# Optimization experiments

Hardware: AMD Instinct MI355X
Metric: run time of the kernel (lower is better)

The kernel has to match this reference:

```python
import jax, jax.numpy as jnp
import numpy as np

B, S, D, DOUT, E = 2, 2048, 1024, 1024, 8
DH = 4 * D  # expert hidden size


def setup_inputs() -> dict:
    key = jax.random.key(0)
    ks = jax.random.split(key, 7)
    sc = lambda *sh: 1.0 / np.sqrt(sh[-2]) if len(sh) >= 2 else 0.02
    return {
        "x": jax.random.normal(ks[0], (B, S, D), jnp.float32),
        "Wg": jax.random.normal(ks[1], (D, E), jnp.float32) / np.sqrt(D),
        "bg": jnp.zeros((E,), jnp.float32),
        "W1": jax.random.normal(ks[2], (E, D, DH), jnp.float32) / np.sqrt(D),
        "b1": jax.random.normal(ks[3], (E, DH), jnp.float32) * 0.02,
        "W2": jax.random.normal(ks[4], (E, DH, DOUT), jnp.float32) / np.sqrt(DH),
        "b2": jax.random.normal(ks[5], (E, DOUT), jnp.float32) * 0.02,
    }


def reference(x, Wg, bg, W1, b1, W2, b2):
    # x: [B, S, D] -> flatten tokens (chunking over seq in the original is
    # math-neutral: routing and expert MLP are per-token).
    Bb, Ss, Dd = x.shape
    xt = x.reshape(-1, Dd)                       # [T, D]
    # Gate: softmax then argmax (top-1 routing, output NOT scaled by gate prob)
    gates = jax.nn.softmax(xt @ Wg + bg, axis=-1)  # [T, E]
    sel = jnp.argmax(gates, axis=-1)               # [T]
    nE = W1.shape[0]
    out = jnp.zeros((xt.shape[0], W2.shape[-1]), x.dtype)
    # Grouped expert MLP expressed as masked dense loop over the small fixed
    # expert count (jit-friendly; a fused gather-grouped-GEMM-scatter kernel
    # is the optimization target).
    for e in range(nE):
        h = jax.nn.gelu(xt @ W1[e] + b1[e], approximate=False)  # [T, 4D]
        ye = h @ W2[e] + b2[e]                                  # [T, DOUT]
        out = jnp.where((sel == e)[:, None], ye, out)
    return out.reshape(Bb, Ss, -1)
```

## Files before the change

### kernel.cpp

```cpp
#include <hip/hip_runtime.h>
#include <hip/hip_bf16.h>
#include <math.h>

#define T_TOK 4096
#define DIM   1024
#define NEXP  8
#define DHID  4096
#define NDOUT 1024
#define BM    128
#define MAXTILES 40

typedef short bf16x8 __attribute__((ext_vector_type(8)));
typedef float f32x4 __attribute__((ext_vector_type(4)));

__device__ __forceinline__ unsigned short f2bf(float f) {
  unsigned u = __float_as_uint(f);
  u += 0x7fffu + ((u >> 16) & 1u);
  return (unsigned short)(u >> 16);
}
__device__ __forceinline__ unsigned pack2bf(float a, float b) {
  return (unsigned)f2bf(a) | ((unsigned)f2bf(b) << 16);
}
__device__ __forceinline__ void gl_lds16(const void* g, void* l) {
  __builtin_amdgcn_global_load_lds(
      (const __attribute__((address_space(1))) void*)g,
      (__attribute__((address_space(3))) void*)l, 16, 0, 0);
}
__device__ __forceinline__ float gelu_fast(float h) {
  float z  = 0.79788456080286536f * (h + 0.044715f * h * h * h);
  float az = fabsf(z);
  float et = __expf(-2.0f * az);
  float th = (1.0f - et) / (1.0f + et);
  th = copysignf(th, z);
  return 0.5f * h * (1.0f + th);
}

__global__ __launch_bounds__(256)
void gate_kernel(const float* __restrict__ x, const float* __restrict__ Wg,
                 const float* __restrict__ bg, int* __restrict__ sel,
                 unsigned short* __restrict__ xbf) {
  int lane = threadIdx.x & 63;
  int wid  = threadIdx.x >> 6;
  int t = blockIdx.x * 4 + wid;
  if (t >= T_TOK) return;
  const float* xr = x + (size_t)t * DIM;
  unsigned short* xbr = xbf + (size_t)t * DIM;
  double acc[NEXP];
#pragma unroll
  for (int e = 0; e < NEXP; e++) acc[e] = 0.0;
#pragma unroll
  for (int j = 0; j < 4; j++) {
    int d0 = j * 256 + lane * 4;
    float4 v = *(const float4*)(xr + d0);
    uint2 p; p.x = pack2bf(v.x, v.y); p.y = pack2bf(v.z, v.w);
    *(uint2*)(xbr + d0) = p;
    float xs[4] = {v.x, v.y, v.z, v.w};
#pragma unroll
    for (int i = 0; i < 4; i++) {
      const float4* wr = reinterpret_cast<const float4*>(Wg + (size_t)(d0 + i) * NEXP);
      float4 w0 = wr[0], w1 = wr[1];
      double xv = (double)xs[i];
      acc[0] += xv * (double)w0.x;
      acc[1] += xv * (double)w0.y;
      acc[2] += xv * (double)w0.z;
      acc[3] += xv * (double)w0.w;
      acc[4] += xv * (double)w1.x;
      acc[5] += xv * (double)w1.y;
      acc[6] += xv * (double)w1.z;
      acc[7] += xv * (double)w1.w;
    }
  }
#pragma unroll
  for (int off = 32; off >= 1; off >>= 1) {
#pragma unroll
    for (int e = 0; e < NEXP; e++) acc[e] += __shfl_down(acc[e], off);
  }
  if (lane == 0) {
    double best = acc[0] + (double)bg[0];
    int bi = 0;
#pragma unroll
    for (int e = 1; e < NEXP; e++) {
      double v = acc[e] + (double)bg[e];
      if (v > best) { best = v; bi = e; }
    }
    sel[t] = bi;
  }
}

__global__ void zero_kernel(int* __restrict__ counts) {
  if (threadIdx.x < NEXP) counts[threadIdx.x] = 0;
}

__global__ void hist_kernel(const int* __restrict__ sel, int* __restrict__ counts) {
  __shared__ int lc[NEXP];
  if (threadIdx.x < NEXP) lc[threadIdx.x] = 0;
  __syncthreads();
  int t = blockIdx.x * 256 + threadIdx.x;
  atomicAdd(&lc[sel[t]], 1);
  __syncthreads();
  if (threadIdx.x < NEXP) atomicAdd(&counts[threadIdx.x], lc[threadIdx.x]);
}

__global__ void plan_kernel(const int* __restrict__ counts, int* __restrict__ base,
                            int* __restrict__ cursor, int* __restrict__ tileExpert,
                            int* __restrict__ tilePos, int* __restrict__ tileRows,
                            int* __restrict__ ntiles) {
  if (threadIdx.x == 0) {
    int acc = 0, nt = 0;
    for (int e = 0; e < NEXP; e++) {
      base[e] = acc; cursor[e] = acc;
      int c = counts[e];
      for (int j = 0; j < c; j += BM) {
        tileExpert[nt] = e;
        tilePos[nt]    = acc + j;
        int rem = c - j;
        tileRows[nt]   = rem < BM ? rem : BM;
        nt++;
      }
      acc += c;
    }
    *ntiles = nt;
  }
}

__global__ void scatter_kernel(const int* __restrict__ sel, int* __restrict__ cursor,
                               int* __restrict__ list) {
  __shared__ int lcnt[NEXP];
  __shared__ int lbase[NEXP];
  int tid = threadIdx.x;
  if (tid < NEXP) lcnt[tid] = 0;
  __syncthreads();
  int t = blockIdx.x * 256 + tid;
  int e = sel[t];
  int lpos = atomicAdd(&lcnt[e], 1);
  __syncthreads();
  if (tid < NEXP) lbase[tid] = atomicAdd(&cursor[tid], lcnt[tid]);
  __syncthreads();
  list[lbase[e] + lpos] = t;
}

__global__ __launch_bounds__(256)
void transpose_tile_kernel(const float* __restrict__ in, unsigned short* __restrict__ out,
                           int K, int N) {
  int nb = blockIdx.x, kb = blockIdx.y, e = blockIdx.z;
  const float* inp = in + (size_t)e * K * N;
  __shared__ unsigned short lds[128][72];
  int tx = threadIdx.x;
  int kloc = tx >> 5;
  int n4   = (tx & 31) << 2;
#pragma unroll
  for (int p = 0; p < 8; p++) {
    int k = p * 8 + kloc;
    float4 v = *(const float4*)(inp + (size_t)(kb * 64 + k) * N + nb * 128 + n4);
    lds[n4 + 0][k] = f2bf(v.x);
    lds[n4 + 1][k] = f2bf(v.y);
    lds[n4 + 2][k] = f2bf(v.z);
    lds[n4 + 3][k] = f2bf(v.w);
  }
  __syncthreads();
  char* tile = (char*)(out + (((size_t)e * gridDim.x + nb) * gridDim.y + kb) * 8192);
  int r  = tx >> 1;
  int kc0 = (tx & 1) * 32;
#pragma unroll
  for (int c = 0; c < 4; c++) {
    int kc = kc0 + c * 8;
    uint4 v = *(const uint4*)&lds[r][kc];
    *(uint4*)(tile + r * 128 + ((2 * kc) ^ ((r & 7) << 4))) = v;
  }
}


__global__ __launch_bounds__(256)
void gemm1_kernel(const unsigned short* __restrict__ xbf, const unsigned short* __restrict__ W1T,
                  const float* __restrict__ b1, const int* __restrict__ list,
                  const int* __restrict__ tileExpert, const int* __restrict__ tilePos,
                  const int* __restrict__ tileRows, const int* __restrict__ ntiles,
                  unsigned short* __restrict__ HcT) {
  int tIdx = blockIdx.y;
  if (tIdx >= *ntiles) return;
  int e = tileExpert[tIdx], posBase = tilePos[tIdx], rows = tileRows[tIdx];
  int nb = blockIdx.x;

  __shared__ __align__(1024) char SH[32768];
  char* As = SH;
  char* Bs = SH + 16384;

  const int tx = threadIdx.x, lane = tx & 63, w = tx >> 6;
  const int wm = w >> 1, wn = w & 1;
  const int rsub = lane >> 3;
  const int px = ((lane & 7) ^ rsub) << 4;

  const char* aS[4];
#pragma unroll
  for (int j = 0; j < 4; j++) {
    int r = w * 32 + j * 8 + rsub;
    int tok = list[posBase + (r < rows ? r : rows - 1)];
    aS[j] = (const char*)xbf + (size_t)tok * (DIM * 2) + px;
  }
  const char* bTile = (const char*)W1T + (((size_t)e * (DHID / 128) + nb) * (DIM / 64)) * 16384
                      + w * 4096 + lane * 16;

  f32x4 acc[4][4];
#pragma unroll
  for (int mf = 0; mf < 4; mf++)
#pragma unroll
    for (int nf = 0; nf < 4; nf++)
      acc[mf][nf] = f32x4{0.f, 0.f, 0.f, 0.f};

  const int NT = DIM / 64;
  for (int kt = 0; kt < NT; kt++) {
#pragma unroll
    for (int j = 0; j < 4; j++) {
      gl_lds16(aS[j] + kt * 128, As + (w * 32 + j * 8) * 128);
      gl_lds16(bTile + kt * 16384 + j * 1024, Bs + w * 4096 + j * 1024);
    }
    __syncthreads();
#pragma unroll
    for (int ks = 0; ks < 2; ks++) {
      int koff = (ks * 64 + (lane >> 4) * 16) ^ ((lane & 7) << 4);
      bf16x8 aF[4], bF[4];
#pragma unroll
      for (int mf = 0; mf < 4; mf++)
        aF[mf] = *(const bf16x8*)(As + (wm * 64 + mf * 16 + (lane & 15)) * 128 + koff);
#pragma unroll
      for (int nf = 0; nf < 4; nf++)
        bF[nf] = *(const bf16x8*)(Bs + (wn * 64 + nf * 16 + (lane & 15)) * 128 + koff);
#pragma unroll
      for (int mf = 0; mf < 4; mf++)
#pragma unroll
        for (int nf = 0; nf < 4; nf++)
          acc[mf][nf] = __builtin_amdgcn_mfma_f32_16x16x32_bf16(aF[mf], bF[nf], acc[mf][nf], 0, 0, 0);
    }
    __syncthreads();
  }

  const float* b1e = b1 + (size_t)e * DHID;
  const int r4 = (lane >> 4) << 2;
  int xj[4];
#pragma unroll
  for (int j = 0; j < 4; j++) xj[j] = ((r4 + j) & 7) << 4;
#pragma unroll
  for (int nf = 0; nf < 4; nf++) {
    int colLoc = wn * 64 + nf * 16 + (lane & 15);
    int tLoc   = colLoc >> 6;
    int k2     = (colLoc & 63) * 2;
    float bias = b1e[nb * 128 + colLoc];
    char* base = SH + tLoc * 16384;
#pragma unroll
    for (int mf = 0; mf < 4; mf++) {
      int rBase = wm * 64 + mf * 16 + r4;
#pragma unroll
      for (int j = 0; j < 4; j++) {
        float g = gelu_fast(acc[mf][nf][j] + bias);
        *(unsigned short*)(base + (rBase + j) * 128 + (k2 ^ xj[j])) = f2bf(g);
      }
    }
  }
  __syncthreads();
  const char* src = SH + tx * 128;
  char* dst = (char*)HcT + (size_t)tIdx * (DHID / 64) * 16384
            + (size_t)(nb * 2 + (tx >> 7)) * 16384 + (tx & 127) * 128;
#pragma unroll
  for (int i = 0; i < 8; i++)
    *(uint4*)(dst + i * 16) = *(const uint4*)(src + i * 16);
}

__global__ __launch_bounds__(256)
void gemm2_kernel(const unsigned short* __restrict__ HcT, const unsigned short* __restrict__ W2T,
                  const float* __restrict__ b2, const int* __restrict__ tileExpert,
                  const int* __restrict__ tilePos, const int* __restrict__ tileRows,
                  const int* __restrict__ ntiles, float* __restrict__ Ppart) {
  int tIdx = blockIdx.y;
  if (tIdx >= *ntiles) return;
  int e = tileExpert[tIdx], posBase = tilePos[tIdx], rows = tileRows[tIdx];
  int nb = blockIdx.x;
  int zs = blockIdx.z;

  __shared__ __align__(1024) char SH[32768];
  char* As = SH;
  char* Bs = SH + 16384;

  const int tx = threadIdx.x, lane = tx & 63, w = tx >> 6;
  const int wm = w >> 1, wn = w & 1;

  const char* aTile = (const char*)HcT + (size_t)tIdx * (DHID / 64) * 16384
                      + (size_t)zs * 32 * 16384 + w * 4096 + lane * 16;
  const char* bTile = (const char*)W2T + (((size_t)e * (NDOUT / 128) + nb) * (DHID / 64)) * 16384
                      + (size_t)zs * 32 * 16384 + w * 4096 + lane * 16;

  f32x4 acc[4][4];
#pragma unroll
  for (int mf = 0; mf < 4; mf++)
#pragma unroll
    for (int nf = 0; nf < 4; nf++)
      acc[mf][nf] = f32x4{0.f, 0.f, 0.f, 0.f};

  const int NT = 32;
  for (int kt = 0; kt < NT; kt++) {
#pragma unroll
    for (int j = 0; j < 4; j++) {
      gl_lds16(aTile + kt * 16384 + j * 1024, As + w * 4096 + j * 1024);
      gl_lds16(bTile + kt * 16384 + j * 1024, Bs + w * 4096 + j * 1024);
    }
    __syncthreads();
#pragma unroll
    for (int ks = 0; ks < 2; ks++) {
      int koff = (ks * 64 + (lane >> 4) * 16) ^ ((lane & 7) << 4);
      bf16x8 aF[4], bF[4];
#pragma unroll
      for (int mf = 0; mf < 4; mf++)
        aF[mf] = *(const bf16x8*)(As + (wm * 64 + mf * 16 + (lane & 15)) * 128 + koff);
#pragma unroll
      for (int nf = 0; nf < 4; nf++)
        bF[nf] = *(const bf16x8*)(Bs + (wn * 64 + nf * 16 + (lane & 15)) * 128 + koff);
#pragma unroll
      for (int mf = 0; mf < 4; mf++)
#pragma unroll
        for (int nf = 0; nf < 4; nf++)
          acc[mf][nf] = __builtin_amdgcn_mfma_f32_16x16x32_bf16(aF[mf], bF[nf], acc[mf][nf], 0, 0, 0);
    }
    __syncthreads();
  }

  const float* b2e = b2 + (size_t)e * NDOUT;
  float* P = Ppart + (size_t)zs * T_TOK * NDOUT;
#pragma unroll
  for (int nf = 0; nf < 4; nf++) {
    int col = nb * 128 + wn * 64 + nf * 16 + (lane & 15);
    float bias = (zs == 0) ? b2e[col] : 0.f;
#pragma unroll
    for (int mf = 0; mf < 4; mf++)
#pragma unroll
      for (int j = 0; j < 4; j++) {
        int rloc = wm * 64 + mf * 16 + ((lane >> 4) << 2) + j;
        if (rloc < rows)
          P[(size_t)(posBase + rloc) * NDOUT + col] = acc[mf][nf][j] + bias;
      }
  }
}

__global__ __launch_bounds__(256)
void reduce_kernel(const float* __restrict__ Ppart, const int* __restrict__ list,
                   float* __restrict__ out) {
  int pos = blockIdx.x;
  int tok = list[pos];
  int c = threadIdx.x * 4;
  float4 a = *(const float4*)(Ppart + (size_t)pos * NDOUT + c);
  float4 b = *(const float4*)(Ppart + (size_t)T_TOK * NDOUT + (size_t)pos * NDOUT + c);
  float4 o; o.x = a.x + b.x; o.y = a.y + b.y; o.z = a.z + b.z; o.w = a.w + b.w;
  *(float4*)(out + (size_t)tok * NDOUT + c) = o;
}

extern "C" void kernel_launch(void* const* d_in, const int* in_sizes, int n_in,
                              void* d_out, int out_size, void* d_ws, size_t ws_size,
                              hipStream_t stream) {
  const float* x  = (const float*)d_in[0];
  const float* Wg = (const float*)d_in[1];
  const float* bg = (const float*)d_in[2];
  const float* W1 = (const float*)d_in[3];
  const float* b1 = (const float*)d_in[4];
  const float* W2 = (const float*)d_in[5];
  const float* b2 = (const float*)d_in[6];
  float* out = (float*)d_out;

  char* ws = (char*)d_ws;
  int* sel        = (int*)(ws);
  int* counts     = (int*)(ws + 16384);
  int* base       = (int*)(ws + 16448);
  int* cursor     = (int*)(ws + 16512);
  int* ntiles     = (int*)(ws + 16576);
  int* tileExpert = (int*)(ws + 16640);
  int* tilePos    = (int*)(ws + 16832);
  int* tileRows   = (int*)(ws + 17024);
  int* list       = (int*)(ws + 17408);

  unsigned short* xbf = (unsigned short*)(ws + (1ull << 20));
  unsigned short* HcT = (unsigned short*)(ws + (10ull << 20));
  unsigned short* W1T = (unsigned short*)(ws + (52ull << 20));
  unsigned short* W2T = (unsigned short*)(ws + (116ull << 20));
  float* Ppart        = (float*)(ws + (52ull << 20));

  gate_kernel<<<T_TOK / 4, 256, 0, stream>>>(x, Wg, bg, sel, xbf);
  zero_kernel<<<1, 64, 0, stream>>>(counts);
  hist_kernel<<<T_TOK / 256, 256, 0, stream>>>(sel, counts);
  plan_kernel<<<1, 64, 0, stream>>>(counts, base, cursor, tileExpert, tilePos, tileRows, ntiles);
  scatter_kernel<<<T_TOK / 256, 256, 0, stream>>>(sel, cursor, list);

  transpose_tile_kernel<<<dim3(DHID / 128, DIM / 64, NEXP), 256, 0, stream>>>(W1, W1T, DIM, DHID);
  transpose_tile_kernel<<<dim3(NDOUT / 128, DHID / 64, NEXP), 256, 0, stream>>>(W2, W2T, DHID, NDOUT);

  gemm1_kernel<<<dim3(DHID / 128, MAXTILES), 256, 0, stream>>>(
      xbf, W1T, b1, list, tileExpert, tilePos, tileRows, ntiles, HcT);
  gemm2_kernel<<<dim3(NDOUT / 128, MAXTILES, 2), 256, 0, stream>>>(
      HcT, W2T, b2, tileExpert, tilePos, tileRows, ntiles, Ppart);
  reduce_kernel<<<T_TOK, 256, 0, stream>>>(Ppart, list, out);
}
```

Baseline: 297.4 us.

## Enlarge grouped GEMM tiles to 256x256 with 1024-thread blocks and 4-way split-K

```diff
diff --git a/kernel.cpp b/kernel.cpp
--- a/kernel.cpp
+++ b/kernel.cpp
@@ -7,8 +7,8 @@
 #define NEXP  8
 #define DHID  4096
 #define NDOUT 1024
-#define BM    128
-#define MAXTILES 40
+#define BM2   256
+#define MAXT  24
 
 typedef short bf16x8 __attribute__((ext_vector_type(8)));
 typedef float f32x4 __attribute__((ext_vector_type(4)));
@@ -110,11 +110,11 @@
     for (int e = 0; e < NEXP; e++) {
       base[e] = acc; cursor[e] = acc;
       int c = counts[e];
-      for (int j = 0; j < c; j += BM) {
+      for (int j = 0; j < c; j += BM2) {
         tileExpert[nt] = e;
         tilePos[nt]    = acc + j;
         int rem = c - j;
-        tileRows[nt]   = rem < BM ? rem : BM;
+        tileRows[nt]   = rem < BM2 ? rem : BM2;
         nt++;
       }
       acc += c;
@@ -170,7 +170,7 @@
 }
 
 
-__global__ __launch_bounds__(256)
+__global__ __launch_bounds__(1024)
 void gemm1_kernel(const unsigned short* __restrict__ xbf, const unsigned short* __restrict__ W1T,
                   const float* __restrict__ b1, const int* __restrict__ list,
                   const int* __restrict__ tileExpert, const int* __restrict__ tilePos,
@@ -181,24 +181,24 @@
   int e = tileExpert[tIdx], posBase = tilePos[tIdx], rows = tileRows[tIdx];
   int nb = blockIdx.x;
 
-  __shared__ __align__(1024) char SH[32768];
+  __shared__ __align__(1024) char SH[65536];
   char* As = SH;
-  char* Bs = SH + 16384;
+  char* Bs = SH + 32768;
 
   const int tx = threadIdx.x, lane = tx & 63, w = tx >> 6;
-  const int wm = w >> 1, wn = w & 1;
-  const int rsub = lane >> 3;
-  const int px = ((lane & 7) ^ rsub) << 4;
-
-  const char* aS[4];
-#pragma unroll
-  for (int j = 0; j < 4; j++) {
-    int r = w * 32 + j * 8 + rsub;
+  const int wm = w >> 2, wn = w & 3;
+
+  const int arow = tx >> 3;
+  const int px = (((tx & 7) ^ (arow & 7)) << 4);
+  const char* aSrc[2];
+#pragma unroll
+  for (int j = 0; j < 2; j++) {
+    int r = arow + j * 128;
     int tok = list[posBase + (r < rows ? r : rows - 1)];
-    aS[j] = (const char*)xbf + (size_t)tok * (DIM * 2) + px;
-  }
-  const char* bTile = (const char*)W1T + (((size_t)e * (DHID / 128) + nb) * (DIM / 64)) * 16384
-                      + w * 4096 + lane * 16;
+    aSrc[j] = (const char*)xbf + (size_t)tok * (DIM * 2) + px;
+  }
+  const char* b0 = (const char*)W1T + ((size_t)(e * 32 + nb * 2) * 16) * 16384 + tx * 16;
+  const char* b1p = b0 + 16 * 16384;
 
   f32x4 acc[4][4];
 #pragma unroll
@@ -209,22 +209,25 @@
 
   const int NT = DIM / 64;
   for (int kt = 0; kt < NT; kt++) {
-#pragma unroll
-    for (int j = 0; j < 4; j++) {
-      gl_lds16(aS[j] + kt * 128, As + (w * 32 + j * 8) * 128);
-      gl_lds16(bTile + kt * 16384 + j * 1024, Bs + w * 4096 + j * 1024);
-    }
+    gl_lds16(aSrc[0] + kt * 128, As + tx * 16);
+    gl_lds16(aSrc[1] + kt * 128, As + 16384 + tx * 16);
+    gl_lds16(b0 + kt * 16384, Bs + tx * 16);
+    gl_lds16(b1p + kt * 16384, Bs + 16384 + tx * 16);
     __syncthreads();
 #pragma unroll
     for (int ks = 0; ks < 2; ks++) {
-      int koff = (ks * 64 + (lane >> 4) * 16) ^ ((lane & 7) << 4);
+      int koff = ks * 64 + ((lane >> 4) << 4);
       bf16x8 aF[4], bF[4];
 #pragma unroll
-      for (int mf = 0; mf < 4; mf++)
-        aF[mf] = *(const bf16x8*)(As + (wm * 64 + mf * 16 + (lane & 15)) * 128 + koff);
-#pragma unroll
-      for (int nf = 0; nf < 4; nf++)
-        bF[nf] = *(const bf16x8*)(Bs + (wn * 64 + nf * 16 + (lane & 15)) * 128 + koff);
+      for (int mf = 0; mf < 4; mf++) {
+        int row = wm * 64 + mf * 16 + (lane & 15);
+        aF[mf] = *(const bf16x8*)(As + row * 128 + (koff ^ ((row & 7) << 4)));
+      }
+#pragma unroll
+      for (int nf = 0; nf < 4; nf++) {
+        int n = wn * 64 + nf * 16 + (lane & 15);
+        bF[nf] = *(const bf16x8*)(Bs + n * 128 + (koff ^ ((n & 7) << 4)));
+      }
 #pragma unroll
       for (int mf = 0; mf < 4; mf++)
 #pragma unroll
@@ -235,37 +238,38 @@
   }
 
   const float* b1e = b1 + (size_t)e * DHID;
-  const int r4 = (lane >> 4) << 2;
-  int xj[4];
-#pragma unroll
-  for (int j = 0; j < 4; j++) xj[j] = ((r4 + j) & 7) << 4;
-#pragma unroll
-  for (int nf = 0; nf < 4; nf++) {
-    int colLoc = wn * 64 + nf * 16 + (lane & 15);
-    int tLoc   = colLoc >> 6;
-    int k2     = (colLoc & 63) * 2;
-    float bias = b1e[nb * 128 + colLoc];
-    char* base = SH + tLoc * 16384;
-#pragma unroll
-    for (int mf = 0; mf < 4; mf++) {
-      int rBase = wm * 64 + mf * 16 + r4;
-#pragma unroll
-      for (int j = 0; j < 4; j++) {
-        float g = gelu_fast(acc[mf][nf][j] + bias);
-        *(unsigned short*)(base + (rBase + j) * 128 + (k2 ^ xj[j])) = f2bf(g);
-      }
-    }
-  }
-  __syncthreads();
-  const char* src = SH + tx * 128;
-  char* dst = (char*)HcT + (size_t)tIdx * (DHID / 64) * 16384
-            + (size_t)(nb * 2 + (tx >> 7)) * 16384 + (tx & 127) * 128;
-#pragma unroll
-  for (int i = 0; i < 8; i++)
-    *(uint4*)(dst + i * 16) = *(const uint4*)(src + i * 16);
-}
-
-__global__ __launch_bounds__(256)
+#pragma unroll
+  for (int p = 0; p < 2; p++) {
+    if ((wn >> 1) == p) {
+      char* region = SH + ((wn & 1) << 15);
+#pragma unroll
+      for (int nf = 0; nf < 4; nf++) {
+        int kloc = nf * 16 + (lane & 15);
+        float bias = b1e[nb * 256 + wn * 64 + kloc];
+#pragma unroll
+        for (int mf = 0; mf < 4; mf++) {
+#pragma unroll
+          for (int j = 0; j < 4; j++) {
+            int row = wm * 64 + mf * 16 + ((lane >> 4) << 2) + j;
+            float g = gelu_fast(acc[mf][nf][j] + bias);
+            *(unsigned short*)(region + row * 128 + ((2 * kloc) ^ ((row & 7) << 4))) = f2bf(g);
+          }
+        }
+      }
+    }
+    __syncthreads();
+    int img = tx >> 9;
+    int off = (tx & 511) * 64;
+    const char* src = SH + img * 32768 + off;
+    char* dst = (char*)HcT + (((size_t)tIdx * 64) + nb * 4 + p * 2 + img) * 32768 + off;
+#pragma unroll
+    for (int i = 0; i < 4; i++)
+      *(uint4*)(dst + i * 16) = *(const uint4*)(src + i * 16);
+    __syncthreads();
+  }
+}
+
+__global__ __launch_bounds__(1024)
 void gemm2_kernel(const unsigned short* __restrict__ HcT, const unsigned short* __restrict__ W2T,
                   const float* __restrict__ b2, const int* __restrict__ tileExpert,
                   const int* __restrict__ tilePos, const int* __restrict__ tileRows,
@@ -276,17 +280,16 @@
   int nb = blockIdx.x;
   int zs = blockIdx.z;
 
-  __shared__ __align__(1024) char SH[32768];
+  __shared__ __align__(1024) char SH[65536];
   char* As = SH;
-  char* Bs = SH + 16384;
+  char* Bs = SH + 32768;
 
   const int tx = threadIdx.x, lane = tx & 63, w = tx >> 6;
-  const int wm = w >> 1, wn = w & 1;
-
-  const char* aTile = (const char*)HcT + (size_t)tIdx * (DHID / 64) * 16384
-                      + (size_t)zs * 32 * 16384 + w * 4096 + lane * 16;
-  const char* bTile = (const char*)W2T + (((size_t)e * (NDOUT / 128) + nb) * (DHID / 64)) * 16384
-                      + (size_t)zs * 32 * 16384 + w * 4096 + lane * 16;
+  const int wm = w >> 2, wn = w & 3;
+
+  const char* aT = (const char*)HcT + ((size_t)tIdx * 64 + zs * 16) * 32768 + tx * 16;
+  const char* b0 = (const char*)W2T + ((size_t)(e * 8 + nb * 2) * 64 + zs * 16) * 16384 + tx * 16;
+  const char* b1p = b0 + 64 * 16384;
 
   f32x4 acc[4][4];
 #pragma unroll
@@ -295,24 +298,27 @@
     for (int nf = 0; nf < 4; nf++)
       acc[mf][nf] = f32x4{0.f, 0.f, 0.f, 0.f};
 
-  const int NT = 32;
+  const int NT = 16;
   for (int kt = 0; kt < NT; kt++) {
-#pragma unroll
-    for (int j = 0; j < 4; j++) {
-      gl_lds16(aTile + kt * 16384 + j * 1024, As + w * 4096 + j * 1024);
-      gl_lds16(bTile + kt * 16384 + j * 1024, Bs + w * 4096 + j * 1024);
-    }
+    gl_lds16(aT + kt * 32768, As + tx * 16);
+    gl_lds16(aT + kt * 32768 + 16384, As + 16384 + tx * 16);
+    gl_lds16(b0 + kt * 16384, Bs + tx * 16);
+    gl_lds16(b1p + kt * 16384, Bs + 16384 + tx * 16);
     __syncthreads();
 #pragma unroll
     for (int ks = 0; ks < 2; ks++) {
-      int koff = (ks * 64 + (lane >> 4) * 16) ^ ((lane & 7) << 4);
+      int koff = ks * 64 + ((lane >> 4) << 4);
       bf16x8 aF[4], bF[4];
 #pragma unroll
-      for (int mf = 0; mf < 4; mf++)
-        aF[mf] = *(const bf16x8*)(As + (wm * 64 + mf * 16 + (lane & 15)) * 128 + koff);
-#pragma unroll
-      for (int nf = 0; nf < 4; nf++)
-        bF[nf] = *(const bf16x8*)(Bs + (wn * 64 + nf * 16 + (lane & 15)) * 128 + koff);
+      for (int mf = 0; mf < 4; mf++) {
+        int row = wm * 64 + mf * 16 + (lane & 15);
+        aF[mf] = *(const bf16x8*)(As + row * 128 + (koff ^ ((row & 7) << 4)));
+      }
+#pragma unroll
+      for (int nf = 0; nf < 4; nf++) {
+        int n = wn * 64 + nf * 16 + (lane & 15);
+        bF[nf] = *(const bf16x8*)(Bs + n * 128 + (koff ^ ((n & 7) << 4)));
+      }
 #pragma unroll
       for (int mf = 0; mf < 4; mf++)
 #pragma unroll
@@ -326,7 +332,7 @@
   float* P = Ppart + (size_t)zs * T_TOK * NDOUT;
 #pragma unroll
   for (int nf = 0; nf < 4; nf++) {
-    int col = nb * 128 + wn * 64 + nf * 16 + (lane & 15);
+    int col = nb * 256 + wn * 64 + nf * 16 + (lane & 15);
     float bias = (zs == 0) ? b2e[col] : 0.f;
 #pragma unroll
     for (int mf = 0; mf < 4; mf++)
@@ -345,10 +351,13 @@
   int pos = blockIdx.x;
   int tok = list[pos];
   int c = threadIdx.x * 4;
-  float4 a = *(const float4*)(Ppart + (size_t)pos * NDOUT + c);
-  float4 b = *(const float4*)(Ppart + (size_t)T_TOK * NDOUT + (size_t)pos * NDOUT + c);
-  float4 o; o.x = a.x + b.x; o.y = a.y + b.y; o.z = a.z + b.z; o.w = a.w + b.w;
-  *(float4*)(out + (size_t)tok * NDOUT + c) = o;
+  float4 s = *(const float4*)(Ppart + (size_t)pos * NDOUT + c);
+#pragma unroll
+  for (int z = 1; z < 4; z++) {
+    float4 a = *(const float4*)(Ppart + (size_t)z * T_TOK * NDOUT + (size_t)pos * NDOUT + c);
+    s.x += a.x; s.y += a.y; s.z += a.z; s.w += a.w;
+  }
+  *(float4*)(out + (size_t)tok * NDOUT + c) = s;
 }
 
 extern "C" void kernel_launch(void* const* d_in, const int* in_sizes, int n_in,
@@ -376,9 +385,9 @@
 
   unsigned short* xbf = (unsigned short*)(ws + (1ull << 20));
   unsigned short* HcT = (unsigned short*)(ws + (10ull << 20));
-  unsigned short* W1T = (unsigned short*)(ws + (52ull << 20));
-  unsigned short* W2T = (unsigned short*)(ws + (116ull << 20));
-  float* Ppart        = (float*)(ws + (52ull << 20));
+  unsigned short* W1T = (unsigned short*)(ws + (58ull << 20));
+  unsigned short* W2T = (unsigned short*)(ws + (122ull << 20));
+  float* Ppart        = (float*)(ws + (58ull << 20));
 
   gate_kernel<<<T_TOK / 4, 256, 0, stream>>>(x, Wg, bg, sel, xbf);
   zero_kernel<<<1, 64, 0, stream>>>(counts);
@@ -389,9 +398,9 @@
   transpose_tile_kernel<<<dim3(DHID / 128, DIM / 64, NEXP), 256, 0, stream>>>(W1, W1T, DIM, DHID);
   transpose_tile_kernel<<<dim3(NDOUT / 128, DHID / 64, NEXP), 256, 0, stream>>>(W2, W2T, DHID, NDOUT);
 
-  gemm1_kernel<<<dim3(DHID / 128, MAXTILES), 256, 0, stream>>>(
+  gemm1_kernel<<<dim3(DHID / 256, MAXT), 1024, 0, stream>>>(
       xbf, W1T, b1, list, tileExpert, tilePos, tileRows, ntiles, HcT);
-  gemm2_kernel<<<dim3(NDOUT / 128, MAXTILES, 2), 256, 0, stream>>>(
+  gemm2_kernel<<<dim3(NDOUT / 256, MAXT, 4), 1024, 0, stream>>>(
       HcT, W2T, b2, tileExpert, tilePos, tileRows, ntiles, Ppart);
   reduce_kernel<<<T_TOK, 256, 0, stream>>>(Ppart, list, out);
 }
```

After: 348.0 us. +17.0%, slower.
